# Optimization experiments

Measured on AMD Instinct MI355X. Metric: run time of the kernel, lower is better.

## Reference

```python
import jax, jax.numpy as jnp
import numpy as np

HIDDEN = 2048
ENGRAM = 256
ENTRIES = 32768
K = 3  # conv kernel size
LN_EPS = 1e-6
NORM_EPS = 1e-8
INV_TEMP = ENGRAM ** 0.5  # retrieval_temperature = 1/sqrt(engram_dim)
CLAMP_MIN = 0.5  # step 0 < clamp_until_step=800 -> hard clamp active


def _l2norm(x):
    n = jnp.linalg.norm(x, axis=-1, keepdims=True)
    return x / jnp.maximum(n, NORM_EPS)


def _rmsnorm(x, w, eps=LN_EPS):
    ms = jnp.mean(jnp.square(x), axis=-1, keepdims=True)
    return x * jax.lax.rsqrt(ms + eps) * w


def _layernorm(x, g, b, eps=LN_EPS):
    mu = jnp.mean(x, axis=-1, keepdims=True)
    var = jnp.mean(jnp.square(x - mu), axis=-1, keepdims=True)
    return (x - mu) * jax.lax.rsqrt(var + eps) * g + b


def setup_inputs() -> dict:
    key = jax.random.key(0)
    ks = jax.random.split(key, 7)
    s = lambda fan: 1.0 / np.sqrt(fan)
    return {
        "hidden_state": jax.random.normal(ks[0], (4, 1024, HIDDEN), jnp.float32),
        "table": jax.random.normal(ks[1], (ENTRIES, ENGRAM), jnp.float32),
        "Wq": jax.random.normal(ks[2], (HIDDEN, ENGRAM), jnp.float32) * s(HIDDEN),
        "ln_gamma": jnp.ones((ENGRAM,), jnp.float32),
        "ln_beta": jnp.zeros((ENGRAM,), jnp.float32),
        "Wk": jax.random.normal(ks[3], (ENGRAM, HIDDEN), jnp.float32) * s(ENGRAM),
        "Wv": jax.random.normal(ks[4], (ENGRAM, HIDDEN), jnp.float32) * s(ENGRAM),
        "gate_norm_w": jnp.ones((HIDDEN,), jnp.float32),
        "key_norm_w": jnp.ones((HIDDEN,), jnp.float32),
        # depthwise causal conv weight [C, K] (torch init zeros; randn for a meaningful test)
        "conv_w": jax.random.normal(ks[5], (HIDDEN, K), jnp.float32) * 0.1,
    }


def reference(hidden_state, table, Wq, ln_gamma, ln_beta, Wk, Wv,
              gate_norm_w, key_norm_w, conv_w):
    B, L, C = hidden_state.shape
    # --- retrieval: cosine-sim softmax attention over frozen table ---
    q = jnp.einsum('blc,ce->ble', hidden_state, Wq)
    qn = _l2norm(q)
    tn = _l2norm(table)
    sims = jnp.einsum('ble,te->blt', qn, tn)            # [B,L,T]
    weights = jax.nn.softmax(sims * INV_TEMP, axis=-1)
    retrieved = jnp.einsum('blt,te->ble', weights, table)
    retrieved = _layernorm(retrieved, ln_gamma, ln_beta)
    # --- key/value projections + gating ---
    key_ = jnp.einsum('ble,ec->blc', retrieved, Wk)
    value = jnp.einsum('ble,ec->blc', retrieved, Wv)
    h_norm = _rmsnorm(hidden_state, gate_norm_w)
    k_norm = _rmsnorm(key_, key_norm_w)
    dot = jnp.sum(h_norm * k_norm, axis=-1, keepdims=True)
    raw_gate = jax.nn.sigmoid(dot / np.sqrt(C).astype(np.float32))
    gate = jnp.maximum(raw_gate, CLAMP_MIN)             # clamp phase (step < 800)
    gated = gate * value                                 # [B,L,C]
    # --- causal depthwise conv along seq (left pad K-1) ---
    padded = jnp.pad(gated, ((0, 0), (K - 1, 0), (0, 0)))
    conv = sum(conv_w[:, k] * padded[:, k:k + L, :] for k in range(K))
    return jax.nn.silu(conv), gate
```

## Files before the change

### kernel.cpp

```cpp
#include <hip/hip_runtime.h>
#include <stdint.h>


#define NTOK 4096
#define CDIM 2048
#define EDIM 256
#define TROWS 32768
#define SPLIT 16
#define OUT0 (NTOK * CDIM)

typedef __attribute__((ext_vector_type(8))) short bf16x8;
typedef __attribute__((ext_vector_type(4))) float f32x4;

__device__ inline float bf2f(unsigned short u) { return __uint_as_float((unsigned)u << 16); }
__device__ inline unsigned short f2bf(float f) {
  unsigned x = __float_as_uint(f);
  x += 0x7fffu + ((x >> 16) & 1u);
  return (unsigned short)(x >> 16);
}
__device__ inline unsigned cvt_pk_bf16(float lo, float hi) {
  unsigned r;
  asm("v_cvt_pk_bf16_f32 %0, %1, %2" : "=v"(r) : "v"(lo), "v"(hi));
  return r;
}
__device__ inline void gll16(const void* g, void* l) {
  __builtin_amdgcn_global_load_lds((const __attribute__((address_space(1))) void*)g,
                                   (__attribute__((address_space(3))) void*)l, 16, 0, 0);
}

__global__ __launch_bounds__(256) void transpose_cast_kernel(
    const float* __restrict__ in0, const float* __restrict__ in1,
    unsigned short* __restrict__ out, int R, int C) {
  __shared__ float lt[32][33];
  const int tid = threadIdx.x;
  const int r0 = blockIdx.x * 32, c0 = blockIdx.y * 32;
  const float* in = blockIdx.z ? in1 : in0;
  unsigned short* op = out + (size_t)blockIdx.z * R * C;
  {
    int r = tid >> 3, c4 = (tid & 7) * 4;
    float4 v = *reinterpret_cast<const float4*>(&in[(size_t)(r0 + r) * C + c0 + c4]);
    lt[r][c4] = v.x; lt[r][c4 + 1] = v.y; lt[r][c4 + 2] = v.z; lt[r][c4 + 3] = v.w;
  }
  __syncthreads();
  {
    int c = tid >> 3, r4 = (tid & 7) * 4;
#pragma unroll
    for (int j = 0; j < 4; ++j)
      op[(size_t)(c0 + c) * R + r0 + r4 + j] = f2bf(lt[r4 + j][c]);
  }
}

__global__ __launch_bounds__(256) void tabprep_kernel(
    const float* __restrict__ table, unsigned short* __restrict__ tnb,
    unsigned short* __restrict__ tvb) {
  __shared__ float lt[32][257];
  __shared__ float inv[32];
  const int tid = threadIdx.x, nb = blockIdx.x;
  const int r0 = nb * 32;
#pragma unroll
  for (int i = 0; i < 8; ++i) {
    int id = i * 256 + tid;
    int row = id >> 6, e4 = (id & 63) * 4;
    float4 v = *reinterpret_cast<const float4*>(&table[(size_t)(r0 + row) * EDIM + e4]);
    lt[row][e4] = v.x; lt[row][e4 + 1] = v.y; lt[row][e4 + 2] = v.z; lt[row][e4 + 3] = v.w;
  }
  __syncthreads();
  {
    int row = tid >> 3, sub = tid & 7;
    float ss = 0.f;
#pragma unroll
    for (int j = 0; j < 32; ++j) { float v = lt[row][sub + 8 * j]; ss = fmaf(v, v, ss); }
    ss += __shfl_xor(ss, 1); ss += __shfl_xor(ss, 2); ss += __shfl_xor(ss, 4);
    if (sub == 0) inv[row] = 1.f / fmaxf(sqrtf(ss), 1e-8f);
  }
  __syncthreads();
#pragma unroll
  for (int i = 0; i < 4; ++i) {
    int q = i * 256 + tid;
    {
      int c8 = q >> 5, row = q & 31;
      bf16x8 v;
#pragma unroll
      for (int j = 0; j < 8; ++j) v[j] = (short)f2bf(lt[row][c8 * 8 + j] * inv[row]);
      *reinterpret_cast<bf16x8*>(&tnb[(size_t)nb * 8192 + q * 8]) = v;
    }
    {
      int hi = q >> 8, e = q & 255;
      bf16x8 v;
#pragma unroll
      for (int j = 0; j < 8; ++j) v[j] = (short)f2bf(lt[hi * 8 + j][e]);
      *reinterpret_cast<bf16x8*>(&tvb[(size_t)nb * 8192 + q * 8]) = v;
    }
  }
}

template <bool F32OUT, bool AF32>
__global__ __launch_bounds__(256, 2) void gemm_bt_kernel(
    const void* __restrict__ Ain, const unsigned short* __restrict__ BT,
    void* __restrict__ Cout, int M, int N, int Kfull, int klen) {
  __shared__ alignas(16) unsigned short sA[2][128 * 64];
  __shared__ alignas(16) unsigned short sB[2][128 * 64];
  const int tid = threadIdx.x;
  const int lane = tid & 63;
  const int wave = tid >> 6;
  const int laneLo = lane & 15, laneHi = lane >> 4;
  const int nbn = N >> 7;
  const int bm = blockIdx.x / nbn, bn = blockIdx.x % nbn;
  const int koff = blockIdx.y * klen;
  const int wr = wave >> 1, wc = wave & 1;
  f32x4 acc[4][4];
#pragma unroll
  for (int m = 0; m < 4; ++m)
#pragma unroll
    for (int n = 0; n < 4; ++n) acc[m][n] = (f32x4){0.f, 0.f, 0.f, 0.f};
  const int nkt = klen >> 6;
  auto STAGE = [&](int b, int kt) {
#pragma unroll
    for (int i = 0; i < 4; ++i) {
      int q = i * 256 + tid;
      int row = q >> 3, cl = q & 7;
      int cs = cl ^ (row & 7);
      if constexpr (AF32) {
        const float* src = (const float*)Ain +
            ((size_t)(bm * 128 + row) * Kfull + koff + kt * 64 + cs * 8);
        float4 x = *reinterpret_cast<const float4*>(src);
        float4 y = *reinterpret_cast<const float4*>(src + 4);
        bf16x8 v;
        v[0] = (short)f2bf(x.x); v[1] = (short)f2bf(x.y);
        v[2] = (short)f2bf(x.z); v[3] = (short)f2bf(x.w);
        v[4] = (short)f2bf(y.x); v[5] = (short)f2bf(y.y);
        v[6] = (short)f2bf(y.z); v[7] = (short)f2bf(y.w);
        *reinterpret_cast<bf16x8*>(&sA[b][q * 8]) = v;
      } else {
        gll16((const unsigned short*)Ain +
                  ((size_t)(bm * 128 + row) * Kfull + koff + kt * 64 + cs * 8),
              &sA[b][q * 8]);
      }
      gll16(BT + ((size_t)(bn * 128 + row) * Kfull + koff + kt * 64 + cs * 8), &sB[b][q * 8]);
    }
  };
  STAGE(0, 0);
  for (int kt = 0; kt < nkt; ++kt) {
    __syncthreads();
    if (kt + 1 < nkt) STAGE((kt & 1) ^ 1, kt + 1);
    const unsigned short* pA = sA[kt & 1];
    const unsigned short* pB = sB[kt & 1];
#pragma unroll
    for (int ks = 0; ks < 2; ++ks) {
      bf16x8 af[4], bfr[4];
#pragma unroll
      for (int m = 0; m < 4; ++m) {
        int row = wr * 64 + m * 16 + laneLo;
        af[m] = *reinterpret_cast<const bf16x8*>(&pA[(row * 8 + ((ks * 4 + laneHi) ^ (row & 7))) * 8]);
      }
#pragma unroll
      for (int n = 0; n < 4; ++n) {
        int row = wc * 64 + n * 16 + laneLo;
        bfr[n] = *reinterpret_cast<const bf16x8*>(&pB[(row * 8 + ((ks * 4 + laneHi) ^ (row & 7))) * 8]);
      }
#pragma unroll
      for (int m = 0; m < 4; ++m)
#pragma unroll
        for (int n = 0; n < 4; ++n)
          acc[m][n] = __builtin_amdgcn_mfma_f32_16x16x32_bf16(af[m], bfr[n], acc[m][n], 0, 0, 0);
    }
  }
#pragma unroll
  for (int m = 0; m < 4; ++m)
#pragma unroll
    for (int n = 0; n < 4; ++n)
#pragma unroll
      for (int r = 0; r < 4; ++r) {
        size_t idx = (size_t)(bm * 128 + wr * 64 + m * 16 + laneHi * 4 + r) * N +
                     bn * 128 + wc * 64 + n * 16 + laneLo;
        if (F32OUT)
          ((float*)Cout)[(size_t)blockIdx.y * M * N + idx] = acc[m][n][r];
        else
          ((unsigned short*)Cout)[idx] = f2bf(acc[m][n][r]);
      }
}

__global__ __launch_bounds__(256) void qcombine_kernel(
    const float* __restrict__ qpart, unsigned short* __restrict__ qn) {
  __shared__ float red[4];
  const int t = blockIdx.x, e = threadIdx.x;
  const int wave = e >> 6, lane = e & 63;
  float v = qpart[(size_t)t * EDIM + e] + qpart[((size_t)NTOK + t) * EDIM + e];
  float ss = v * v;
#pragma unroll
  for (int m = 1; m <= 32; m <<= 1) ss += __shfl_xor(ss, m);
  if (lane == 0) red[wave] = ss;
  __syncthreads();
  ss = red[0] + red[1] + red[2] + red[3];
  const float inv = 1.f / fmaxf(sqrtf(ss), 1e-8f);
  qn[(size_t)t * EDIM + e] = f2bf(v * inv);
}

__global__ __launch_bounds__(256, 2) void attn_kernel(
    const unsigned short* __restrict__ qn, const unsigned short* __restrict__ tnb,
    const unsigned short* __restrict__ tvb, unsigned short* __restrict__ Opart,
    float* __restrict__ lpart) {
  __shared__ alignas(16) unsigned short bufK[2][8192];
  __shared__ alignas(16) unsigned short bufV[2][8192];
  __shared__ alignas(16) unsigned short pbuf[8][16][40];
  const int tid = threadIdx.x;
  const int wave = tid >> 6, lane = tid & 63;
  const int Lo = lane & 15, Hi = lane >> 4;
  const int cid = (blockIdx.x & 7) * 64 + (blockIdx.x >> 3);
  const int split = cid >> 5, tb = cid & 31;
  const int qkBase = tb * 128 + wave * 32;
  bf16x8 qf[2][8];
#pragma unroll
  for (int g = 0; g < 2; ++g)
#pragma unroll
    for (int ks = 0; ks < 8; ++ks)
      qf[g][ks] = *reinterpret_cast<const bf16x8*>(
          qn + (size_t)(qkBase + g * 16 + Lo) * EDIM + ks * 32 + Hi * 8);
  const int pvG = (wave & 1) * 4;
  const int pvF = (wave >> 1) * 8;
  f32x4 o[4][8];
#pragma unroll
  for (int ng = 0; ng < 4; ++ng)
#pragma unroll
    for (int f = 0; f < 8; ++f) o[ng][f] = (f32x4){0.f, 0.f, 0.f, 0.f};
  float l_run[2] = {0.f, 0.f};
  const int nt = (TROWS / SPLIT) / 32;
  const int nb0 = split * nt;
  auto STAGE_K = [&](int b, int blk) {
#pragma unroll
    for (int i = 0; i < 4; ++i) {
      int u = i * 256 + tid;
      gll16(tnb + (size_t)blk * 8192 + u * 8, &bufK[b][u * 8]);
    }
  };
  auto STAGE_V = [&](int b, int blk) {
#pragma unroll
    for (int i = 0; i < 4; ++i) {
      int u = i * 256 + tid;
      gll16(tvb + (size_t)blk * 8192 + u * 8, &bufV[b][u * 8]);
    }
  };
  auto PV = [&](const unsigned short* vb0) {
    bf16x8 pa0 = *reinterpret_cast<const bf16x8*>(&pbuf[pvG + 0][Lo][Hi * 8]);
    bf16x8 pa1 = *reinterpret_cast<const bf16x8*>(&pbuf[pvG + 1][Lo][Hi * 8]);
    bf16x8 pa2 = *reinterpret_cast<const bf16x8*>(&pbuf[pvG + 2][Lo][Hi * 8]);
    bf16x8 pa3 = *reinterpret_cast<const bf16x8*>(&pbuf[pvG + 3][Lo][Hi * 8]);
#pragma unroll
    for (int f = 0; f < 8; ++f) {
      bf16x8 vb = *reinterpret_cast<const bf16x8*>(
          &vb0[(Hi * 256 + (pvF + f) * 16 + Lo) * 8]);
      o[0][f] = __builtin_amdgcn_mfma_f32_16x16x32_bf16(pa0, vb, o[0][f], 0, 0, 0);
      o[1][f] = __builtin_amdgcn_mfma_f32_16x16x32_bf16(pa1, vb, o[1][f], 0, 0, 0);
      o[2][f] = __builtin_amdgcn_mfma_f32_16x16x32_bf16(pa2, vb, o[2][f], 0, 0, 0);
      o[3][f] = __builtin_amdgcn_mfma_f32_16x16x32_bf16(pa3, vb, o[3][f], 0, 0, 0);
    }
  };
  STAGE_K(0, nb0);
  for (int it = 0; it < nt; ++it) {
    const int cur = it & 1;
    __syncthreads();
    if (it + 1 < nt) STAGE_K(cur ^ 1, nb0 + it + 1);
    STAGE_V(cur ^ 1, nb0 + it);
    f32x4 z00 = {0.f, 0.f, 0.f, 0.f}, z01 = z00, z10 = z00, z11 = z00;
    __builtin_amdgcn_s_setprio(1);
#pragma unroll
    for (int ks = 0; ks < 8; ++ks) {
      bf16x8 a0 = *reinterpret_cast<const bf16x8*>(&bufK[cur][((ks * 4 + Hi) * 32 + Lo) * 8]);
      bf16x8 a1 = *reinterpret_cast<const bf16x8*>(&bufK[cur][((ks * 4 + Hi) * 32 + 16 + Lo) * 8]);
      z00 = __builtin_amdgcn_mfma_f32_16x16x32_bf16(a0, qf[0][ks], z00, 0, 0, 0);
      z01 = __builtin_amdgcn_mfma_f32_16x16x32_bf16(a1, qf[0][ks], z01, 0, 0, 0);
      z10 = __builtin_amdgcn_mfma_f32_16x16x32_bf16(a0, qf[1][ks], z10, 0, 0, 0);
      z11 = __builtin_amdgcn_mfma_f32_16x16x32_bf16(a1, qf[1][ks], z11, 0, 0, 0);
    }
    __builtin_amdgcn_s_setprio(0);
    uint2 pw[2][2];
#pragma unroll
    for (int g = 0; g < 2; ++g) {
      const f32x4 za = g ? z10 : z00;
      const f32x4 zb = g ? z11 : z01;
      float p[8];
#pragma unroll
      for (int r = 0; r < 4; ++r) {
        p[r] = __expf(fmaf(16.f, za[r], -16.f));
        p[4 + r] = __expf(fmaf(16.f, zb[r], -16.f));
      }
      l_run[g] += ((p[0] + p[1]) + (p[2] + p[3])) + ((p[4] + p[5]) + (p[6] + p[7]));
      pw[g][0] = make_uint2(cvt_pk_bf16(p[0], p[1]), cvt_pk_bf16(p[2], p[3]));
      pw[g][1] = make_uint2(cvt_pk_bf16(p[4], p[5]), cvt_pk_bf16(p[6], p[7]));
    }
    if (it > 0) {
      __builtin_amdgcn_s_setprio(1);
      PV(bufV[cur]);
      __builtin_amdgcn_s_setprio(0);
    }
    asm volatile("s_waitcnt lgkmcnt(0)\n\ts_barrier" ::: "memory");
#pragma unroll
    for (int g = 0; g < 2; ++g) {
      unsigned short* pb = &pbuf[wave * 2 + g][Lo][0];
      *reinterpret_cast<uint2*>(pb + Hi * 4) = pw[g][0];
      *reinterpret_cast<uint2*>(pb + 16 + Hi * 4) = pw[g][1];
    }
  }
  __syncthreads();
  __builtin_amdgcn_s_setprio(1);
  PV(bufV[nt & 1]);
  __builtin_amdgcn_s_setprio(0);
#pragma unroll
  for (int g = 0; g < 2; ++g) {
    float l = l_run[g];
    l += __shfl_xor(l, 16);
    l += __shfl_xor(l, 32);
    if (lane < 16) lpart[(size_t)split * NTOK + qkBase + g * 16 + Lo] = l;
  }
#pragma unroll
  for (int ng = 0; ng < 4; ++ng)
#pragma unroll
    for (int f = 0; f < 8; ++f)
#pragma unroll
      for (int r = 0; r < 4; ++r) {
        int token = tb * 128 + (pvG + ng) * 16 + Hi * 4 + r;
        Opart[((size_t)split * NTOK + token) * EDIM + (pvF + f) * 16 + Lo] =
            f2bf(o[ng][f][r]);
      }
}

__global__ __launch_bounds__(256) void combine_ln_kernel(
    const unsigned short* __restrict__ Opart, const float* __restrict__ lpart,
    const float* __restrict__ gamma, const float* __restrict__ beta,
    unsigned short* __restrict__ retr) {
  __shared__ float red[4][2];
  const int t = blockIdx.x, e = threadIdx.x;
  const int wave = e >> 6, lane = e & 63;
  float acc = 0.f, l = 0.f;
#pragma unroll
  for (int s = 0; s < SPLIT; ++s) {
    acc += bf2f(Opart[((size_t)s * NTOK + t) * EDIM + e]);
    l += lpart[(size_t)s * NTOK + t];
  }
  const float r = acc / l;
  float s1 = r, s2 = r * r;
#pragma unroll
  for (int m = 1; m <= 32; m <<= 1) { s1 += __shfl_xor(s1, m); s2 += __shfl_xor(s2, m); }
  if (lane == 0) { red[wave][0] = s1; red[wave][1] = s2; }
  __syncthreads();
  s1 = red[0][0] + red[1][0] + red[2][0] + red[3][0];
  s2 = red[0][1] + red[1][1] + red[2][1] + red[3][1];
  const float mu = s1 * (1.f / 256.f);
  const float var = s2 * (1.f / 256.f) - mu * mu;
  const float rs = rsqrtf(var + 1e-6f);
  retr[(size_t)t * EDIM + e] = f2bf((r - mu) * rs * gamma[e] + beta[e]);
}

__global__ __launch_bounds__(256) void gate_kernel(
    const float* __restrict__ hidden, const unsigned short* __restrict__ kv,
    const float* __restrict__ gw, const float* __restrict__ kwn,
    float* __restrict__ gate_out) {
  __shared__ float red[4][3];
  const int t = blockIdx.x, tid = threadIdx.x;
  const int wave = tid >> 6, lane = tid & 63;
  float ssh = 0.f, ssk = 0.f, shk = 0.f;
#pragma unroll
  for (int i = 0; i < 8; ++i) {
    int cc = tid + i * 256;
    float h = hidden[(size_t)t * CDIM + cc];
    float k = bf2f(kv[(size_t)t * 4096 + cc]);
    ssh = fmaf(h, h, ssh);
    ssk = fmaf(k, k, ssk);
    shk = fmaf(h * gw[cc], k * kwn[cc], shk);
  }
#pragma unroll
  for (int m = 1; m <= 32; m <<= 1) {
    ssh += __shfl_xor(ssh, m); ssk += __shfl_xor(ssk, m); shk += __shfl_xor(shk, m);
  }
  if (lane == 0) { red[wave][0] = ssh; red[wave][1] = ssk; red[wave][2] = shk; }
  __syncthreads();
  ssh = red[0][0] + red[1][0] + red[2][0] + red[3][0];
  ssk = red[0][1] + red[1][1] + red[2][1] + red[3][1];
  shk = red[0][2] + red[1][2] + red[2][2] + red[3][2];
  const float rsh = rsqrtf(ssh * (1.f / 2048.f) + 1e-6f);
  const float rsk = rsqrtf(ssk * (1.f / 2048.f) + 1e-6f);
  const float dot = rsh * rsk * shk;
  const float rg = 1.f / (1.f + __expf(-dot * 0.02209708691207961f));
  if (tid == 0) gate_out[t] = fmaxf(rg, 0.5f);
}

__global__ __launch_bounds__(256) void conv_kernel(
    const unsigned short* __restrict__ kv, const float* __restrict__ gate,
    const float* __restrict__ convw, float* __restrict__ out0) {
  const int bid = blockIdx.x, tid = threadIdx.x;
  const int t = (bid & 7) * 512 + (bid >> 3);
  const int l = t & 1023;
  const int c0 = tid * 8;
  const float gt2 = gate[t];
  const float gt1 = (l >= 1) ? gate[t - 1] : 0.f;
  const float gt0 = (l >= 2) ? gate[t - 2] : 0.f;
  bf16x8 vz;
#pragma unroll
  for (int j = 0; j < 8; ++j) vz[j] = 0;
  const unsigned short* vbase = kv + 2048;
  bf16x8 v2 = *reinterpret_cast<const bf16x8*>(vbase + (size_t)t * 4096 + c0);
  bf16x8 v1 = (l >= 1) ? *reinterpret_cast<const bf16x8*>(vbase + (size_t)(t - 1) * 4096 + c0) : vz;
  bf16x8 v0 = (l >= 2) ? *reinterpret_cast<const bf16x8*>(vbase + (size_t)(t - 2) * 4096 + c0) : vz;
  float res[8];
#pragma unroll
  for (int j = 0; j < 8; ++j) {
    int c = c0 + j;
    float x = convw[c * 3 + 0] * (gt0 * bf2f((unsigned short)v0[j]))
            + convw[c * 3 + 1] * (gt1 * bf2f((unsigned short)v1[j]))
            + convw[c * 3 + 2] * (gt2 * bf2f((unsigned short)v2[j]));
    res[j] = x / (1.f + __expf(-x));
  }
  *reinterpret_cast<float4*>(out0 + (size_t)t * CDIM + c0) =
      make_float4(res[0], res[1], res[2], res[3]);
  *reinterpret_cast<float4*>(out0 + (size_t)t * CDIM + c0 + 4) =
      make_float4(res[4], res[5], res[6], res[7]);
}

extern "C" void kernel_launch(void* const* d_in, const int* in_sizes, int n_in,
                              void* d_out, int out_size, void* d_ws, size_t ws_size,
                              hipStream_t stream) {
  const float* hidden = (const float*)d_in[0];
  const float* table  = (const float*)d_in[1];
  const float* Wq     = (const float*)d_in[2];
  const float* ln_g   = (const float*)d_in[3];
  const float* ln_b   = (const float*)d_in[4];
  const float* Wk     = (const float*)d_in[5];
  const float* Wv     = (const float*)d_in[6];
  const float* gnw    = (const float*)d_in[7];
  const float* knw    = (const float*)d_in[8];
  const float* convw  = (const float*)d_in[9];
  float* out = (float*)d_out;

  char* w = (char*)d_ws;
  const size_t MB = 1u << 20;
  unsigned short* tnb    = (unsigned short*)(w);
  unsigned short* tvb    = (unsigned short*)(w + 16 * MB);
  unsigned short* kv     = (unsigned short*)(w);
  unsigned short* qn     = (unsigned short*)(w + 32 * MB);
  unsigned short* retr   = (unsigned short*)(w + 32 * MB);
  unsigned short* WkvT   = (unsigned short*)(w + 34 * MB);
  float*          lpart  = (float*)(w + 36 * MB);
  unsigned short* Opart  = (unsigned short*)(w + 37 * MB);
  unsigned short* WqT    = (unsigned short*)(w + 53 * MB);
  float*          qpart  = (float*)(w + 54 * MB);

  transpose_cast_kernel<<<dim3(64, 8, 1), 256, 0, stream>>>(Wq, Wq, WqT, CDIM, EDIM);
  transpose_cast_kernel<<<dim3(8, 64, 2), 256, 0, stream>>>(Wk, Wv, WkvT, EDIM, CDIM);
  tabprep_kernel<<<TROWS / 32, 256, 0, stream>>>(table, tnb, tvb);
  gemm_bt_kernel<true, true><<<dim3((NTOK / 128) * (EDIM / 128), 2), 256, 0, stream>>>(
      hidden, WqT, qpart, NTOK, EDIM, CDIM, 1024);
  qcombine_kernel<<<NTOK, 256, 0, stream>>>(qpart, qn);
  attn_kernel<<<32 * SPLIT, 256, 0, stream>>>(qn, tnb, tvb, Opart, lpart);
  combine_ln_kernel<<<NTOK, 256, 0, stream>>>(Opart, lpart, ln_g, ln_b, retr);
  gemm_bt_kernel<false, false><<<dim3((NTOK / 128) * (2 * CDIM / 128), 1), 256, 0, stream>>>(
      retr, WkvT, kv, NTOK, 2 * CDIM, EDIM, EDIM);
  gate_kernel<<<NTOK, 256, 0, stream>>>(hidden, kv, gnw, knw, out + OUT0);
  conv_kernel<<<NTOK, 256, 0, stream>>>(kv, out + OUT0, convw, out);
}
```

Before: 226.6 us.

## Remove skewed PV pipeline in attention loop and merge weight transpose launches

The attention loop previously ran PV one iteration behind QK, staging V separately and overlapping PV of the prior block with QK and exp of the current one. It now stages K and V together, writes P straight to LDS, barriers, and runs PV on the current block in the same iteration, dropping the software skew and the tail PV. This simplifies the schedule and register use but removes the overlap between PV MFMAs and the softmax and exp work. Separately, the two weight transpose-cast launches are merged into one 3D grid with early exit for out-of-range tiles, which launches many idle blocks.

```diff
diff --git a/kernel.cpp b/kernel.cpp
--- a/kernel.cpp
+++ b/kernel.cpp
@@ -29,13 +29,18 @@
 }
 
 __global__ __launch_bounds__(256) void transpose_cast_kernel(
-    const float* __restrict__ in0, const float* __restrict__ in1,
-    unsigned short* __restrict__ out, int R, int C) {
+    const float* __restrict__ Wq, const float* __restrict__ Wk,
+    const float* __restrict__ Wv, unsigned short* __restrict__ WqT,
+    unsigned short* __restrict__ WkvT) {
   __shared__ float lt[32][33];
+  const int z = blockIdx.z;
+  const float* in = z == 0 ? Wq : (z == 1 ? Wk : Wv);
+  unsigned short* op = z == 0 ? WqT : (WkvT + (size_t)(z - 1) * CDIM * EDIM);
+  const int R = z == 0 ? CDIM : EDIM;
+  const int C = z == 0 ? EDIM : CDIM;
+  const int r0 = blockIdx.x * 32, c0 = blockIdx.y * 32;
+  if (r0 >= R || c0 >= C) return;
   const int tid = threadIdx.x;
-  const int r0 = blockIdx.x * 32, c0 = blockIdx.y * 32;
-  const float* in = blockIdx.z ? in1 : in0;
-  unsigned short* op = out + (size_t)blockIdx.z * R * C;
   {
     int r = tid >> 3, c4 = (tid & 7) * 4;
     float4 v = *reinterpret_cast<const float4*>(&in[(size_t)(r0 + r) * C + c0 + c4]);
@@ -226,41 +231,19 @@
   float l_run[2] = {0.f, 0.f};
   const int nt = (TROWS / SPLIT) / 32;
   const int nb0 = split * nt;
-  auto STAGE_K = [&](int b, int blk) {
+  auto STAGE = [&](int b, int blk) {
 #pragma unroll
     for (int i = 0; i < 4; ++i) {
       int u = i * 256 + tid;
       gll16(tnb + (size_t)blk * 8192 + u * 8, &bufK[b][u * 8]);
+      gll16(tvb + (size_t)blk * 8192 + u * 8, &bufV[b][u * 8]);
     }
   };
-  auto STAGE_V = [&](int b, int blk) {
-#pragma unroll
-    for (int i = 0; i < 4; ++i) {
-      int u = i * 256 + tid;
-      gll16(tvb + (size_t)blk * 8192 + u * 8, &bufV[b][u * 8]);
-    }
-  };
-  auto PV = [&](const unsigned short* vb0) {
-    bf16x8 pa0 = *reinterpret_cast<const bf16x8*>(&pbuf[pvG + 0][Lo][Hi * 8]);
-    bf16x8 pa1 = *reinterpret_cast<const bf16x8*>(&pbuf[pvG + 1][Lo][Hi * 8]);
-    bf16x8 pa2 = *reinterpret_cast<const bf16x8*>(&pbuf[pvG + 2][Lo][Hi * 8]);
-    bf16x8 pa3 = *reinterpret_cast<const bf16x8*>(&pbuf[pvG + 3][Lo][Hi * 8]);
-#pragma unroll
-    for (int f = 0; f < 8; ++f) {
-      bf16x8 vb = *reinterpret_cast<const bf16x8*>(
-          &vb0[(Hi * 256 + (pvF + f) * 16 + Lo) * 8]);
-      o[0][f] = __builtin_amdgcn_mfma_f32_16x16x32_bf16(pa0, vb, o[0][f], 0, 0, 0);
-      o[1][f] = __builtin_amdgcn_mfma_f32_16x16x32_bf16(pa1, vb, o[1][f], 0, 0, 0);
-      o[2][f] = __builtin_amdgcn_mfma_f32_16x16x32_bf16(pa2, vb, o[2][f], 0, 0, 0);
-      o[3][f] = __builtin_amdgcn_mfma_f32_16x16x32_bf16(pa3, vb, o[3][f], 0, 0, 0);
-    }
-  };
-  STAGE_K(0, nb0);
+  STAGE(0, nb0);
   for (int it = 0; it < nt; ++it) {
     const int cur = it & 1;
     __syncthreads();
-    if (it + 1 < nt) STAGE_K(cur ^ 1, nb0 + it + 1);
-    STAGE_V(cur ^ 1, nb0 + it);
+    if (it + 1 < nt) STAGE(cur ^ 1, nb0 + it + 1);
     f32x4 z00 = {0.f, 0.f, 0.f, 0.f}, z01 = z00, z10 = z00, z11 = z00;
     __builtin_amdgcn_s_setprio(1);
 #pragma unroll
@@ -273,7 +256,6 @@
       z11 = __builtin_amdgcn_mfma_f32_16x16x32_bf16(a1, qf[1][ks], z11, 0, 0, 0);
     }
     __builtin_amdgcn_s_setprio(0);
-    uint2 pw[2][2];
 #pragma unroll
     for (int g = 0; g < 2; ++g) {
       const f32x4 za = g ? z10 : z00;
@@ -285,26 +267,29 @@
         p[4 + r] = __expf(fmaf(16.f, zb[r], -16.f));
       }
       l_run[g] += ((p[0] + p[1]) + (p[2] + p[3])) + ((p[4] + p[5]) + (p[6] + p[7]));
-      pw[g][0] = make_uint2(cvt_pk_bf16(p[0], p[1]), cvt_pk_bf16(p[2], p[3]));
-      pw[g][1] = make_uint2(cvt_pk_bf16(p[4], p[5]), cvt_pk_bf16(p[6], p[7]));
-    }
-    if (it > 0) {
-      __builtin_amdgcn_s_setprio(1);
-      PV(bufV[cur]);
-      __builtin_amdgcn_s_setprio(0);
+      unsigned short* pb = &pbuf[wave * 2 + g][Lo][0];
+      *reinterpret_cast<uint2*>(pb + Hi * 4) =
+          make_uint2(cvt_pk_bf16(p[0], p[1]), cvt_pk_bf16(p[2], p[3]));
+      *reinterpret_cast<uint2*>(pb + 16 + Hi * 4) =
+          make_uint2(cvt_pk_bf16(p[4], p[5]), cvt_pk_bf16(p[6], p[7]));
     }
     asm volatile("s_waitcnt lgkmcnt(0)\n\ts_barrier" ::: "memory");
-#pragma unroll
-    for (int g = 0; g < 2; ++g) {
-      unsigned short* pb = &pbuf[wave * 2 + g][Lo][0];
-      *reinterpret_cast<uint2*>(pb + Hi * 4) = pw[g][0];
-      *reinterpret_cast<uint2*>(pb + 16 + Hi * 4) = pw[g][1];
-    }
-  }
-  __syncthreads();
-  __builtin_amdgcn_s_setprio(1);
-  PV(bufV[nt & 1]);
-  __builtin_amdgcn_s_setprio(0);
+    bf16x8 pa0 = *reinterpret_cast<const bf16x8*>(&pbuf[pvG + 0][Lo][Hi * 8]);
+    bf16x8 pa1 = *reinterpret_cast<const bf16x8*>(&pbuf[pvG + 1][Lo][Hi * 8]);
+    bf16x8 pa2 = *reinterpret_cast<const bf16x8*>(&pbuf[pvG + 2][Lo][Hi * 8]);
+    bf16x8 pa3 = *reinterpret_cast<const bf16x8*>(&pbuf[pvG + 3][Lo][Hi * 8]);
+    __builtin_amdgcn_s_setprio(1);
+#pragma unroll
+    for (int f = 0; f < 8; ++f) {
+      bf16x8 vb = *reinterpret_cast<const bf16x8*>(
+          &bufV[cur][(Hi * 256 + (pvF + f) * 16 + Lo) * 8]);
+      o[0][f] = __builtin_amdgcn_mfma_f32_16x16x32_bf16(pa0, vb, o[0][f], 0, 0, 0);
+      o[1][f] = __builtin_amdgcn_mfma_f32_16x16x32_bf16(pa1, vb, o[1][f], 0, 0, 0);
+      o[2][f] = __builtin_amdgcn_mfma_f32_16x16x32_bf16(pa2, vb, o[2][f], 0, 0, 0);
+      o[3][f] = __builtin_amdgcn_mfma_f32_16x16x32_bf16(pa3, vb, o[3][f], 0, 0, 0);
+    }
+    __builtin_amdgcn_s_setprio(0);
+  }
 #pragma unroll
   for (int g = 0; g < 2; ++g) {
     float l = l_run[g];
@@ -444,8 +429,7 @@
   unsigned short* WqT    = (unsigned short*)(w + 53 * MB);
   float*          qpart  = (float*)(w + 54 * MB);
 
-  transpose_cast_kernel<<<dim3(64, 8, 1), 256, 0, stream>>>(Wq, Wq, WqT, CDIM, EDIM);
-  transpose_cast_kernel<<<dim3(8, 64, 2), 256, 0, stream>>>(Wk, Wv, WkvT, EDIM, CDIM);
+  transpose_cast_kernel<<<dim3(64, 64, 3), 256, 0, stream>>>(Wq, Wk, Wv, WqT, WkvT);
   tabprep_kernel<<<TROWS / 32, 256, 0, stream>>>(table, tnb, tvb);
   gemm_bt_kernel<true, true><<<dim3((NTOK / 128) * (EDIM / 128), 2), 256, 0, stream>>>(
       hidden, WqT, qpart, NTOK, EDIM, CDIM, 1024);
```

Measured after the change: 222.3 us. About the same (-1.9%).
